# Kernel optimization log

Measured on AMD Instinct MI355X. Metric: run time of the kernel, lower is better.

The kernel has to match this reference:

```python
import jax, jax.numpy as jnp
import numpy as np

N = 50000      # nodes
E = 800000     # edges (avg degree 16)
NF, EF, H, OUT, K = 16, 8, 64, 8, 3
N_MID = 2      # n_gnn_layers=4 -> first + 2 mid + last


def setup_inputs() -> dict:
    key = jax.random.key(0)
    ks = jax.random.split(key, 16)
    s = 0.05
    return {
        "x": jax.random.normal(ks[0], (N, NF), dtype=jnp.float32),
        "edge_index": jax.random.randint(ks[1], (2, E), 0, N, dtype=jnp.int64),
        "edge_attr": jax.random.normal(ks[2], (E, EF), dtype=jnp.float32),
        # edge_aggr MLP: Linear(EF,H) -> ReLU -> Linear(H,1)
        "mlp_W1": jax.random.normal(ks[3], (EF, H), dtype=jnp.float32) * s,
        "mlp_b1": jnp.zeros((H,), dtype=jnp.float32),
        "mlp_W2": jax.random.normal(ks[4], (H, 1), dtype=jnp.float32) * s,
        "mlp_b2": jnp.zeros((1,), dtype=jnp.float32),
        # TAGConv-style layers: K+1 linear maps each
        "W_first": jax.random.normal(ks[5], (K + 1, NF, H), dtype=jnp.float32) * s,
        "b_first": jnp.zeros((H,), dtype=jnp.float32),
        "W_mid": jax.random.normal(ks[6], (N_MID, K + 1, H, H), dtype=jnp.float32) * s,
        "b_mid": jnp.zeros((N_MID, H), dtype=jnp.float32),
        "W_last": jax.random.normal(ks[7], (K + 1, H, OUT), dtype=jnp.float32) * s,
        "b_last": jnp.zeros((OUT,), dtype=jnp.float32),
    }


def _gcn_norm(edge_weight, src, dst, n_nodes):
    # deg computed at target (col), D^{-1/2} A D^{-1/2}, no self loops
    deg = jax.ops.segment_sum(edge_weight, dst, num_segments=n_nodes)
    dinv = jnp.where(deg > 0, jax.lax.rsqrt(jnp.where(deg > 0, deg, 1.0)), 0.0)
    return dinv[src] * edge_weight * dinv[dst]  # [E]


def _tag_conv(x, Ws, b, src, dst, norm, n_nodes):
    # out = sum_k (A_norm^k x) W_k + b
    out = x @ Ws[0]
    h = x
    for k in range(1, Ws.shape[0]):
        h = jax.ops.segment_sum(h[src] * norm[:, None], dst, num_segments=n_nodes)
        out = out + h @ Ws[k]
    return out + b


def reference(x, edge_index, edge_attr, mlp_W1, mlp_b1, mlp_W2, mlp_b2,
              W_first, b_first, W_mid, b_mid, W_last, b_last):
    src, dst = edge_index[0], edge_index[1]
    n_nodes = x.shape[0]
    # edge MLP -> scalar edge weight per edge
    ew = (jax.nn.relu(edge_attr @ mlp_W1 + mlp_b1) @ mlp_W2 + mlp_b2)[:, 0]  # [E]
    norm = _gcn_norm(ew, src, dst, n_nodes)
    h = jax.nn.relu(_tag_conv(x, W_first, b_first, src, dst, norm, n_nodes))
    for i in range(W_mid.shape[0]):
        h = jax.nn.relu(_tag_conv(h, W_mid[i], b_mid[i], src, dst, norm, n_nodes))
    return _tag_conv(h, W_last, b_last, src, dst, norm, n_nodes)
```

## Files before the change

kernel.cpp:

```cpp
#include <hip/hip_runtime.h>
#include <stdint.h>

#define N_NODES 50000
#define N_EDGES 800000
#define NFEAT   16
#define EFEAT   8
#define HID     64
#define OUTF    8
#define NMID    2
#define NX      (N_NODES * NFEAT)
#define NPW     16
#define CAP     64
#define PGB     ((N_NODES + 4 * NPW - 1) / (4 * NPW))
#define PPB     ((N_NODES + 15) / 16)
#define NWB     ((N_NODES + 3) / 4)

typedef unsigned short ushort_t;
typedef unsigned int   uint_t;
typedef unsigned long long ull_t;
typedef __bf16 bf16x8 __attribute__((ext_vector_type(8)));
typedef float  f32x4  __attribute__((ext_vector_type(4)));

__device__ __forceinline__ float b2f(ushort_t u) {
    return __uint_as_float(((uint_t)u) << 16);
}
__device__ __forceinline__ ushort_t f2b(float f) {
    uint_t u = __float_as_uint(f);
    return (ushort_t)((u + 0x7fffu + ((u >> 16) & 1u)) >> 16);
}
__device__ __forceinline__ float h2f(ushort_t u) {
    union { ushort_t u; _Float16 h; } c; c.u = u; return (float)c.h;
}
__device__ __forceinline__ ushort_t f2h(float f) {
    union { ushort_t u; _Float16 h; } c; c.h = (_Float16)f; return c.u;
}

__global__ __launch_bounds__(256) void edge_mlp_kernel(
    const float* __restrict__ ea, const float* __restrict__ x,
    const int* __restrict__ ei,
    const float* __restrict__ W1, const float* __restrict__ b1,
    const float* __restrict__ W2, const float* __restrict__ b2,
    ushort_t* __restrict__ xb,
    int* __restrict__ cnts, ull_t* __restrict__ bucket8)
{
    int tid = threadIdx.x;
    int e = blockIdx.x * 256 + tid;
    if (e >= N_EDGES) return;

    int d = ei[N_EDGES + e];
    int pos = atomicAdd(&cnts[d], 1);
    int sn = ei[e];

    xb[e] = f2b(x[e]);

    float4 v0 = ((const float4*)ea)[2 * e];
    float4 v1 = ((const float4*)ea)[2 * e + 1];
    float a[8] = {v0.x, v0.y, v0.z, v0.w, v1.x, v1.y, v1.z, v1.w};

    float h[HID];
    #pragma unroll
    for (int j = 0; j < HID; ++j) h[j] = b1[j];

    #pragma unroll
    for (int i = 0; i < EFEAT; ++i) {
        float ai = a[i];
        #pragma unroll
        for (int j = 0; j < HID; ++j)
            h[j] = fmaf(ai, W1[i * HID + j], h[j]);
    }

    float acc = b2[0];
    #pragma unroll
    for (int j = 0; j < HID; ++j)
        acc = fmaf(fmaxf(h[j], 0.f), W2[j], acc);

    if (pos < CAP)
        bucket8[(size_t)d * CAP + pos] =
            (((ull_t)__float_as_uint(acc)) << 32) | (uint_t)sn;
}

__global__ __launch_bounds__(256) void degdinv_kernel(
    int* __restrict__ cnts, const ull_t* __restrict__ bucket8,
    float* __restrict__ dinv)
{
    int tid = threadIdx.x;
    int n = blockIdx.x * 4 + (tid >> 6);
    int lane = tid & 63;
    if (n >= N_NODES) return;
    int c = cnts[n]; if (c > CAP) c = CAP;
    float w = 0.f;
    if (lane < c)
        w = __uint_as_float((uint_t)(bucket8[(size_t)n * CAP + lane] >> 32));
    #pragma unroll
    for (int o = 32; o; o >>= 1) w += __shfl_down(w, o, 64);
    if (lane == 0) {
        cnts[n] = c;
        dinv[n] = (w > 0.f) ? (1.f / sqrtf(w)) : 0.f;
    }
}

__global__ __launch_bounds__(256) void rescale_kernel(
    const int* __restrict__ cnts, const float* __restrict__ dinv,
    const ull_t* __restrict__ bucket8, uint_t* __restrict__ bucket4)
{
    int tid = threadIdx.x;
    int n = blockIdx.x * 4 + (tid >> 6);
    int lane = tid & 63;
    if (n >= N_NODES) return;
    int c = cnts[n];
    float dn = dinv[n];
    if (lane < c) {
        ull_t q = bucket8[(size_t)n * CAP + lane];
        uint_t s = (uint_t)q;
        float ewv = __uint_as_float((uint_t)(q >> 32));
        float nv = dinv[s] * ewv * dn;
        nv = fminf(fmaxf(nv, -60000.f), 60000.f);
        bucket4[(size_t)n * CAP + lane] = (((uint_t)f2h(nv)) << 16) | s;
    }
}

template<int W>
__global__ __launch_bounds__(256, 6) void prop_kernel(
    const ushort_t* __restrict__ gsrc, ushort_t* __restrict__ gout,
    const int* __restrict__ cnts, const uint_t* __restrict__ bucket)
{
    int tid = threadIdx.x;
    int wv = tid >> 6, lane = tid & 63;
    int nb = (blockIdx.x * 4 + wv) * 4;
    if (nb >= N_NODES) return;

    int cv = (lane < 4) ? cnts[nb + lane] : 0;
    int c0 = __builtin_amdgcn_readlane(cv, 0);
    int c1 = __builtin_amdgcn_readlane(cv, 1);
    int c2 = __builtin_amdgcn_readlane(cv, 2);
    int c3 = __builtin_amdgcn_readlane(cv, 3);
    int cm = max(max(c0, c1), max(c2, c3));

    uint_t p0 = 0, p1 = 0, p2 = 0, p3 = 0;
    if (lane < c0) p0 = bucket[(size_t)(nb + 0) * CAP + lane];
    if (lane < c1) p1 = bucket[(size_t)(nb + 1) * CAP + lane];
    if (lane < c2) p2 = bucket[(size_t)(nb + 2) * CAP + lane];
    if (lane < c3) p3 = bucket[(size_t)(nb + 3) * CAP + lane];

    if (W == 64) {
        float s[4][4];
        #pragma unroll
        for (int n = 0; n < 4; ++n)
            #pragma unroll
            for (int k = 0; k < 4; ++k) s[n][k] = 0.f;

        for (int j = 0; j < cm; j += 4) {
            float hv[4][4], nv[4][4];
            #pragma unroll
            for (int k = 0; k < 4; ++k) {
                int pe0 = __builtin_amdgcn_readlane((int)p0, j + k);
                int pe1 = __builtin_amdgcn_readlane((int)p1, j + k);
                int pe2 = __builtin_amdgcn_readlane((int)p2, j + k);
                int pe3 = __builtin_amdgcn_readlane((int)p3, j + k);
                nv[0][k] = h2f((ushort_t)(((uint_t)pe0) >> 16));
                nv[1][k] = h2f((ushort_t)(((uint_t)pe1) >> 16));
                nv[2][k] = h2f((ushort_t)(((uint_t)pe2) >> 16));
                nv[3][k] = h2f((ushort_t)(((uint_t)pe3) >> 16));
                hv[0][k] = b2f(gsrc[(size_t)(pe0 & 0xffff) * 64 + lane]);
                hv[1][k] = b2f(gsrc[(size_t)(pe1 & 0xffff) * 64 + lane]);
                hv[2][k] = b2f(gsrc[(size_t)(pe2 & 0xffff) * 64 + lane]);
                hv[3][k] = b2f(gsrc[(size_t)(pe3 & 0xffff) * 64 + lane]);
            }
            #pragma unroll
            for (int n = 0; n < 4; ++n)
                #pragma unroll
                for (int k = 0; k < 4; ++k)
                    s[n][k] = fmaf(hv[n][k], nv[n][k], s[n][k]);
        }

        #pragma unroll
        for (int n = 0; n < 4; ++n) {
            float v = (s[n][0] + s[n][1]) + (s[n][2] + s[n][3]);
            gout[(size_t)(nb + n) * 64 + lane] = f2b(v);
        }
    } else {
        const int il = lane & 15;
        const int quad = lane >> 4;
        float s0 = 0.f, s1 = 0.f, s2 = 0.f, s3 = 0.f;

        #pragma unroll 2
        for (int j = 0; j < cm; j += 4) {
            int jq = j + quad;
            int w0 = __shfl((int)p0, jq, 64);
            int w1 = __shfl((int)p1, jq, 64);
            int w2 = __shfl((int)p2, jq, 64);
            int w3 = __shfl((int)p3, jq, 64);
            float h0 = b2f(gsrc[(size_t)(w0 & 0xffff) * 16 + il]);
            float h1 = b2f(gsrc[(size_t)(w1 & 0xffff) * 16 + il]);
            float h2 = b2f(gsrc[(size_t)(w2 & 0xffff) * 16 + il]);
            float h3 = b2f(gsrc[(size_t)(w3 & 0xffff) * 16 + il]);
            s0 = fmaf(h0, h2f((ushort_t)(((uint_t)w0) >> 16)), s0);
            s1 = fmaf(h1, h2f((ushort_t)(((uint_t)w1) >> 16)), s1);
            s2 = fmaf(h2, h2f((ushort_t)(((uint_t)w2) >> 16)), s2);
            s3 = fmaf(h3, h2f((ushort_t)(((uint_t)w3) >> 16)), s3);
        }

        s0 += __shfl_xor(s0, 16, 64); s0 += __shfl_xor(s0, 32, 64);
        s1 += __shfl_xor(s1, 16, 64); s1 += __shfl_xor(s1, 32, 64);
        s2 += __shfl_xor(s2, 16, 64); s2 += __shfl_xor(s2, 32, 64);
        s3 += __shfl_xor(s3, 16, 64); s3 += __shfl_xor(s3, 32, 64);
        if (lane < 16) {
            gout[(size_t)(nb + 0) * 16 + lane] = f2b(s0);
            gout[(size_t)(nb + 1) * 16 + lane] = f2b(s1);
            gout[(size_t)(nb + 2) * 16 + lane] = f2b(s2);
            gout[(size_t)(nb + 3) * 16 + lane] = f2b(s3);
        }
    }
}

template<int F32OUT>
__global__ __launch_bounds__(256, 8) void prop8_kernel(
    const ushort_t* __restrict__ gsrc, int GS, int GO,
    const ushort_t* __restrict__ add, int AS, int AO,
    ushort_t* __restrict__ outb, float* __restrict__ outf,
    const int* __restrict__ cnts, const uint_t* __restrict__ bucket)
{
    int tid = threadIdx.x;
    int wv = tid >> 6, lane = tid & 63;
    int nb = (blockIdx.x * 4 + wv) * 4;
    if (nb >= N_NODES) return;
    const int oct = lane >> 3, il = lane & 7;

    int cv = (lane < 4) ? cnts[nb + lane] : 0;
    int c0 = __builtin_amdgcn_readlane(cv, 0);
    int c1 = __builtin_amdgcn_readlane(cv, 1);
    int c2 = __builtin_amdgcn_readlane(cv, 2);
    int c3 = __builtin_amdgcn_readlane(cv, 3);
    int cm = max(max(c0, c1), max(c2, c3));

    uint_t p0 = 0, p1 = 0, p2 = 0, p3 = 0;
    if (lane < c0) p0 = bucket[(size_t)(nb + 0) * CAP + lane];
    if (lane < c1) p1 = bucket[(size_t)(nb + 1) * CAP + lane];
    if (lane < c2) p2 = bucket[(size_t)(nb + 2) * CAP + lane];
    if (lane < c3) p3 = bucket[(size_t)(nb + 3) * CAP + lane];

    float s0 = 0.f, s1 = 0.f, s2 = 0.f, s3 = 0.f;

    #pragma unroll 2
    for (int j = 0; j < cm; j += 8) {
        int jo = j + oct;
        int w0 = __shfl((int)p0, jo, 64);
        int w1 = __shfl((int)p1, jo, 64);
        int w2 = __shfl((int)p2, jo, 64);
        int w3 = __shfl((int)p3, jo, 64);
        float h0 = b2f(gsrc[(size_t)(w0 & 0xffff) * GS + GO + il]);
        float h1 = b2f(gsrc[(size_t)(w1 & 0xffff) * GS + GO + il]);
        float h2 = b2f(gsrc[(size_t)(w2 & 0xffff) * GS + GO + il]);
        float h3 = b2f(gsrc[(size_t)(w3 & 0xffff) * GS + GO + il]);
        s0 = fmaf(h0, h2f((ushort_t)(((uint_t)w0) >> 16)), s0);
        s1 = fmaf(h1, h2f((ushort_t)(((uint_t)w1) >> 16)), s1);
        s2 = fmaf(h2, h2f((ushort_t)(((uint_t)w2) >> 16)), s2);
        s3 = fmaf(h3, h2f((ushort_t)(((uint_t)w3) >> 16)), s3);
    }

    #define FIN(sN, n)                                                               \
        {                                                                            \
            float s = sN;                                                            \
            s += __shfl_xor(s, 8, 64);                                               \
            s += __shfl_xor(s, 16, 64);                                              \
            s += __shfl_xor(s, 32, 64);                                              \
            if (lane < 8) {                                                          \
                float v = s + b2f(add[(size_t)(nb + n) * AS + AO + lane]);           \
                if (F32OUT) outf[(size_t)(nb + n) * 8 + lane] = v;                   \
                else        outb[(size_t)(nb + n) * 8 + lane] = f2b(v);              \
            }                                                                        \
        }
    FIN(s0, 0)
    FIN(s1, 1)
    FIN(s2, 2)
    FIN(s3, 3)
    #undef FIN
}

template<int SRCW, int COUT, int ACT>
__global__ __launch_bounds__(256, 4) void gemm4_kernel(
    const ushort_t* __restrict__ s0, const ushort_t* __restrict__ s1,
    const ushort_t* __restrict__ s2, const ushort_t* __restrict__ s3,
    const float* __restrict__ Wg,
    const float* __restrict__ bias,
    ushort_t* __restrict__ outb)
{
    constexpr int NCH = (SRCW == 16) ? 2 : 8;
    constexpr int NT  = (COUT + 15) / 16;
    __shared__ __align__(16) ushort_t Bp[NCH * NT * 512];

    int tid = threadIdx.x;
    for (int idx = tid; idx < NCH * NT * 512; idx += 256) {
        int f = idx >> 9;
        int l = (idx >> 3) & 63, j = idx & 7;
        int ch = f / NT, nt = f - ch * NT;
        int kk = ((l >> 4) << 3) + j;
        int n = nt * 16 + (l & 15);
        int widx, krow;
        if (SRCW == 16) { widx = 2 * ch + (kk >> 4); krow = kk & 15; }
        else            { widx = ch >> 1;            krow = ((ch & 1) << 5) + kk; }
        float v = (n < COUT) ? Wg[((size_t)widx * SRCW + krow) * COUT + n] : 0.f;
        Bp[idx] = f2b(v);
    }
    __syncthreads();

    int wv = tid >> 6, lane = tid & 63;
    int node_base = (blockIdx.x * 4 + wv) * NPW;
    if (node_base >= N_NODES) return;
    int m = lane & 15, quad = lane >> 4;

    const ushort_t* srcs[4] = {s0, s1, s2, s3};
    bf16x8 a[NCH];
    #pragma unroll
    for (int ch = 0; ch < NCH; ++ch) {
        const ushort_t* sp;
        size_t off;
        if (SRCW == 16) {
            sp = (quad < 2) ? srcs[2 * ch] : srcs[2 * ch + 1];
            off = (size_t)(node_base + m) * 16 + (quad & 1) * 8;
        } else {
            sp = srcs[ch >> 1];
            off = (size_t)(node_base + m) * 64 + ((ch & 1) << 5) + quad * 8;
        }
        a[ch] = *(const bf16x8*)(sp + off);
    }

    #pragma unroll
    for (int nt = 0; nt < NT; ++nt) {
        float bv = bias[(nt * 16 + m) & (COUT - 1)];
        f32x4 c = {bv, bv, bv, bv};
        #pragma unroll
        for (int ch = 0; ch < NCH; ++ch) {
            bf16x8 b = *(const bf16x8*)&Bp[((ch * NT + nt) * 64 + lane) * 8];
            c = __builtin_amdgcn_mfma_f32_16x16x32_bf16(a[ch], b, c, 0, 0, 0);
        }
        #pragma unroll
        for (int r = 0; r < 4; ++r) {
            int row = node_base + quad * 4 + r;
            float v = ACT ? fmaxf(c[r], 0.f) : c[r];
            outb[(size_t)row * COUT + nt * 16 + m] = f2b(v);
        }
    }
}

__global__ __launch_bounds__(256, 4) void gemmL_kernel(
    const ushort_t* __restrict__ src,
    const float* __restrict__ Wl,
    const float* __restrict__ bl,
    ushort_t* __restrict__ Z)
{
    __shared__ __align__(16) ushort_t Bp[2 * 2 * 512];

    int tid = threadIdx.x;
    for (int idx = tid; idx < 2048; idx += 256) {
        int f = idx >> 9;
        int ch = f >> 1, nt = f & 1;
        int l = (idx >> 3) & 63, j = idx & 7;
        int kg = ch * 32 + ((l >> 4) << 3) + j;
        int n = nt * 16 + (l & 15);
        int widx = n >> 3, col = n & 7;
        Bp[idx] = f2b(Wl[((size_t)widx * 64 + kg) * 8 + col]);
    }
    __syncthreads();

    int wv = tid >> 6, lane = tid & 63;
    int node_base = (blockIdx.x * 4 + wv) * NPW;
    if (node_base >= N_NODES) return;
    int m = lane & 15, quad = lane >> 4;

    bf16x8 a[2];
    #pragma unroll
    for (int ch = 0; ch < 2; ++ch)
        a[ch] = *(const bf16x8*)(src + (size_t)(node_base + m) * 64 + ch * 32 + quad * 8);

    #pragma unroll
    for (int nt = 0; nt < 2; ++nt) {
        int n = nt * 16 + m;
        float bv = (n < 8) ? bl[n] : 0.f;
        f32x4 c = {bv, bv, bv, bv};
        #pragma unroll
        for (int ch = 0; ch < 2; ++ch) {
            bf16x8 b = *(const bf16x8*)&Bp[((ch * 2 + nt) * 64 + lane) * 8];
            c = __builtin_amdgcn_mfma_f32_16x16x32_bf16(a[ch], b, c, 0, 0, 0);
        }
        #pragma unroll
        for (int r = 0; r < 4; ++r) {
            int row = node_base + quad * 4 + r;
            Z[(size_t)row * 32 + n] = f2b(c[r]);
        }
    }
}

extern "C" void kernel_launch(void* const* d_in, const int* in_sizes, int n_in,
                              void* d_out, int out_size, void* d_ws, size_t ws_size,
                              hipStream_t stream)
{
    const float* x  = (const float*)d_in[0];
    const int*   ei = (const int*)d_in[1];
    const float* ea = (const float*)d_in[2];
    const float* W1 = (const float*)d_in[3];
    const float* b1 = (const float*)d_in[4];
    const float* W2 = (const float*)d_in[5];
    const float* b2 = (const float*)d_in[6];
    const float* Wf = (const float*)d_in[7];
    const float* bf = (const float*)d_in[8];
    const float* Wm = (const float*)d_in[9];
    const float* bm = (const float*)d_in[10];
    const float* Wl = (const float*)d_in[11];
    const float* bl = (const float*)d_in[12];

    char* ws = (char*)d_ws;
    size_t off = 0;
    auto take = [&](size_t bytes) -> char* {
        char* p = ws + off;
        off = (off + bytes + 255) & ~(size_t)255;
        return p;
    };
    int*      cnts    = (int*)take((size_t)N_NODES * 4);
    float*    dinv    = (float*)take((size_t)N_NODES * 4);
    ull_t*    bucket8 = (ull_t*)take((size_t)N_NODES * CAP * 8);
    uint_t*   bucket4 = (uint_t*)take((size_t)N_NODES * CAP * 4);
    ushort_t* xb      = (ushort_t*)take((size_t)NX * 2 + 256);
    ushort_t* g1      = (ushort_t*)take((size_t)N_NODES * HID * 2 + 256);
    ushort_t* g2      = (ushort_t*)take((size_t)N_NODES * HID * 2 + 256);
    ushort_t* g3      = (ushort_t*)take((size_t)N_NODES * HID * 2 + 256);
    ushort_t* curA    = (ushort_t*)take((size_t)N_NODES * HID * 2 + 256);
    ushort_t* curB    = (ushort_t*)take((size_t)N_NODES * HID * 2 + 256);
    ushort_t* Z       = (ushort_t*)take((size_t)N_NODES * 32 * 2 + 256);
    ushort_t* t8a     = (ushort_t*)take((size_t)N_NODES * 8 * 2 + 256);
    ushort_t* t8b     = (ushort_t*)take((size_t)N_NODES * 8 * 2 + 256);

    hipMemsetAsync(cnts, 0, (size_t)N_NODES * 4, stream);

    const int EB = (N_EDGES + 255) / 256;

    edge_mlp_kernel<<<EB, 256, 0, stream>>>(ea, x, ei, W1, b1, W2, b2, xb, cnts, bucket8);
    degdinv_kernel<<<NWB, 256, 0, stream>>>(cnts, bucket8, dinv);
    rescale_kernel<<<NWB, 256, 0, stream>>>(cnts, dinv, bucket8, bucket4);

    prop_kernel<NFEAT><<<PPB, 256, 0, stream>>>(xb, g1, cnts, bucket4);
    prop_kernel<NFEAT><<<PPB, 256, 0, stream>>>(g1, g2, cnts, bucket4);
    prop_kernel<NFEAT><<<PPB, 256, 0, stream>>>(g2, g3, cnts, bucket4);
    gemm4_kernel<NFEAT, HID, 1><<<PGB, 256, 0, stream>>>(
        xb, g1, g2, g3, Wf, bf, curA);

    ushort_t* cin = curA;
    ushort_t* cot = curB;
    for (int L = 0; L < NMID; ++L) {
        prop_kernel<HID><<<PPB, 256, 0, stream>>>(cin, g1, cnts, bucket4);
        prop_kernel<HID><<<PPB, 256, 0, stream>>>(g1, g2, cnts, bucket4);
        prop_kernel<HID><<<PPB, 256, 0, stream>>>(g2, g3, cnts, bucket4);
        gemm4_kernel<HID, HID, 1><<<PGB, 256, 0, stream>>>(
            cin, g1, g2, g3, Wm + (size_t)L * 4 * HID * HID, bm + L * HID, cot);
        ushort_t* t = cin; cin = cot; cot = t;
    }

    gemmL_kernel<<<PGB, 256, 0, stream>>>(cin, Wl, bl, Z);
    prop8_kernel<0><<<PPB, 256, 0, stream>>>(Z, 32, 24, Z, 32, 16, t8a, nullptr, cnts, bucket4);
    prop8_kernel<0><<<PPB, 256, 0, stream>>>(t8a, 8, 0, Z, 32, 8, t8b, nullptr, cnts, bucket4);
    prop8_kernel<1><<<PPB, 256, 0, stream>>>(t8b, 8, 0, Z, 32, 0, nullptr, (float*)d_out, cnts, bucket4);
}
```

Baseline: 414.4 us.

## Restructure prop kernel lanes to gather 4 bf16 columns per lane

Rewrites the propagation kernel's lane mapping so each 16-lane group of a wave handles one of the four nodes. Each lane gathers 4 bf16 features with one 8-byte vector load, and bucket entries are spread across lanes and broadcast by shuffle instead of readlane. The aim is fewer, wider gather loads and less per-edge scalar overhead. The W=16 path also changes its reduction pattern. The occupancy hint in launch_bounds is dropped. The cost is a per-node serial loop bounded by the wave's max degree, and possible register growth without the occupancy hint.

```diff
diff --git a/kernel.cpp b/kernel.cpp
--- a/kernel.cpp
+++ b/kernel.cpp
@@ -120,7 +120,7 @@
 }
 
 template<int W>
-__global__ __launch_bounds__(256, 6) void prop_kernel(
+__global__ __launch_bounds__(256) void prop_kernel(
     const ushort_t* __restrict__ gsrc, ushort_t* __restrict__ gout,
     const int* __restrict__ cnts, const uint_t* __restrict__ bucket)
 {
@@ -129,86 +129,114 @@
     int nb = (blockIdx.x * 4 + wv) * 4;
     if (nb >= N_NODES) return;
 
+    int nsel = lane >> 4;
     int cv = (lane < 4) ? cnts[nb + lane] : 0;
     int c0 = __builtin_amdgcn_readlane(cv, 0);
     int c1 = __builtin_amdgcn_readlane(cv, 1);
     int c2 = __builtin_amdgcn_readlane(cv, 2);
     int c3 = __builtin_amdgcn_readlane(cv, 3);
     int cm = max(max(c0, c1), max(c2, c3));
-
-    uint_t p0 = 0, p1 = 0, p2 = 0, p3 = 0;
-    if (lane < c0) p0 = bucket[(size_t)(nb + 0) * CAP + lane];
-    if (lane < c1) p1 = bucket[(size_t)(nb + 1) * CAP + lane];
-    if (lane < c2) p2 = bucket[(size_t)(nb + 2) * CAP + lane];
-    if (lane < c3) p3 = bucket[(size_t)(nb + 3) * CAP + lane];
+    int cmy = (nsel == 0) ? c0 : (nsel == 1) ? c1 : (nsel == 2) ? c2 : c3;
+
+    int es = lane & 15;
+    const uint_t* bb = bucket + (size_t)(nb + nsel) * CAP + es;
+    uint_t q0 = (es      < cmy) ? bb[0]  : 0u;
+    uint_t q1 = (es + 16 < cmy) ? bb[16] : 0u;
+    uint_t q2 = (es + 32 < cmy) ? bb[32] : 0u;
+    uint_t q3 = (es + 48 < cmy) ? bb[48] : 0u;
+
+    int bidx = lane & 48;
 
     if (W == 64) {
-        float s[4][4];
-        #pragma unroll
-        for (int n = 0; n < 4; ++n)
+        const int colg = (lane & 15) * 4;
+        const ushort_t* gbase = gsrc + colg;
+        float s0 = 0.f, s1 = 0.f, s2 = 0.f, s3 = 0.f;
+
+        #define STEP64(QR, T)                                                        \
+            {                                                                        \
+                int w = __shfl((int)QR, bidx + (T), 64);                             \
+                float nv = h2f((ushort_t)(((uint_t)w) >> 16));                       \
+                uint2 d = *(const uint2*)(gbase + (size_t)(w & 0xffff) * 64);        \
+                s0 = fmaf(__uint_as_float(d.x << 16), nv, s0);                       \
+                s1 = fmaf(__uint_as_float(d.x & 0xffff0000u), nv, s1);               \
+                s2 = fmaf(__uint_as_float(d.y << 16), nv, s2);                       \
+                s3 = fmaf(__uint_as_float(d.y & 0xffff0000u), nv, s3);               \
+            }
+
+        {
+            int lim = cm < 16 ? cm : 16;
+            #pragma unroll 4
+            for (int t = 0; t < lim; ++t) STEP64(q0, t)
+        }
+        if (cm > 16) {
+            int lim = cm - 16; if (lim > 16) lim = 16;
+            #pragma unroll 4
+            for (int t = 0; t < lim; ++t) STEP64(q1, t)
+        }
+        if (cm > 32) {
+            int lim = cm - 32; if (lim > 16) lim = 16;
+            #pragma unroll 4
+            for (int t = 0; t < lim; ++t) STEP64(q2, t)
+        }
+        if (cm > 48) {
+            int lim = cm - 48; if (lim > 16) lim = 16;
+            #pragma unroll 4
+            for (int t = 0; t < lim; ++t) STEP64(q3, t)
+        }
+        #undef STEP64
+
+        uint2 o;
+        o.x = (uint_t)f2b(s0) | (((uint_t)f2b(s1)) << 16);
+        o.y = (uint_t)f2b(s2) | (((uint_t)f2b(s3)) << 16);
+        *(uint2*)(gout + (size_t)(nb + nsel) * 64 + colg) = o;
+    } else {
+        const int qg = (lane >> 2) & 3;
+        const int colg = (lane & 3) * 4;
+        const ushort_t* gbase = gsrc + colg;
+        float s0 = 0.f, s1 = 0.f, s2 = 0.f, s3 = 0.f;
+
+        #define STEP16(QR, T)                                                        \
+            {                                                                        \
+                int w = __shfl((int)QR, bidx + (T) + qg, 64);                        \
+                float nv = h2f((ushort_t)(((uint_t)w) >> 16));                       \
+                uint2 d = *(const uint2*)(gbase + (size_t)(w & 0xffff) * 16);        \
+                s0 = fmaf(__uint_as_float(d.x << 16), nv, s0);                       \
+                s1 = fmaf(__uint_as_float(d.x & 0xffff0000u), nv, s1);               \
+                s2 = fmaf(__uint_as_float(d.y << 16), nv, s2);                       \
+                s3 = fmaf(__uint_as_float(d.y & 0xffff0000u), nv, s3);               \
+            }
+
+        {
+            int lim = cm < 16 ? cm : 16;
             #pragma unroll
-            for (int k = 0; k < 4; ++k) s[n][k] = 0.f;
-
-        for (int j = 0; j < cm; j += 4) {
-            float hv[4][4], nv[4][4];
+            for (int t = 0; t < 16; t += 4) { if (t < lim) STEP16(q0, t) }
+        }
+        if (cm > 16) {
+            int lim = cm - 16; if (lim > 16) lim = 16;
             #pragma unroll
-            for (int k = 0; k < 4; ++k) {
-                int pe0 = __builtin_amdgcn_readlane((int)p0, j + k);
-                int pe1 = __builtin_amdgcn_readlane((int)p1, j + k);
-                int pe2 = __builtin_amdgcn_readlane((int)p2, j + k);
-                int pe3 = __builtin_amdgcn_readlane((int)p3, j + k);
-                nv[0][k] = h2f((ushort_t)(((uint_t)pe0) >> 16));
-                nv[1][k] = h2f((ushort_t)(((uint_t)pe1) >> 16));
-                nv[2][k] = h2f((ushort_t)(((uint_t)pe2) >> 16));
-                nv[3][k] = h2f((ushort_t)(((uint_t)pe3) >> 16));
-                hv[0][k] = b2f(gsrc[(size_t)(pe0 & 0xffff) * 64 + lane]);
-                hv[1][k] = b2f(gsrc[(size_t)(pe1 & 0xffff) * 64 + lane]);
-                hv[2][k] = b2f(gsrc[(size_t)(pe2 & 0xffff) * 64 + lane]);
-                hv[3][k] = b2f(gsrc[(size_t)(pe3 & 0xffff) * 64 + lane]);
-            }
+            for (int t = 0; t < 16; t += 4) { if (t < lim) STEP16(q1, t) }
+        }
+        if (cm > 32) {
+            int lim = cm - 32; if (lim > 16) lim = 16;
             #pragma unroll
-            for (int n = 0; n < 4; ++n)
-                #pragma unroll
-                for (int k = 0; k < 4; ++k)
-                    s[n][k] = fmaf(hv[n][k], nv[n][k], s[n][k]);
-        }
-
-        #pragma unroll
-        for (int n = 0; n < 4; ++n) {
-            float v = (s[n][0] + s[n][1]) + (s[n][2] + s[n][3]);
-            gout[(size_t)(nb + n) * 64 + lane] = f2b(v);
-        }
-    } else {
-        const int il = lane & 15;
-        const int quad = lane >> 4;
-        float s0 = 0.f, s1 = 0.f, s2 = 0.f, s3 = 0.f;
-
-        #pragma unroll 2
-        for (int j = 0; j < cm; j += 4) {
-            int jq = j + quad;
-            int w0 = __shfl((int)p0, jq, 64);
-            int w1 = __shfl((int)p1, jq, 64);
-            int w2 = __shfl((int)p2, jq, 64);
-            int w3 = __shfl((int)p3, jq, 64);
-            float h0 = b2f(gsrc[(size_t)(w0 & 0xffff) * 16 + il]);
-            float h1 = b2f(gsrc[(size_t)(w1 & 0xffff) * 16 + il]);
-            float h2 = b2f(gsrc[(size_t)(w2 & 0xffff) * 16 + il]);
-            float h3 = b2f(gsrc[(size_t)(w3 & 0xffff) * 16 + il]);
-            s0 = fmaf(h0, h2f((ushort_t)(((uint_t)w0) >> 16)), s0);
-            s1 = fmaf(h1, h2f((ushort_t)(((uint_t)w1) >> 16)), s1);
-            s2 = fmaf(h2, h2f((ushort_t)(((uint_t)w2) >> 16)), s2);
-            s3 = fmaf(h3, h2f((ushort_t)(((uint_t)w3) >> 16)), s3);
-        }
-
-        s0 += __shfl_xor(s0, 16, 64); s0 += __shfl_xor(s0, 32, 64);
-        s1 += __shfl_xor(s1, 16, 64); s1 += __shfl_xor(s1, 32, 64);
-        s2 += __shfl_xor(s2, 16, 64); s2 += __shfl_xor(s2, 32, 64);
-        s3 += __shfl_xor(s3, 16, 64); s3 += __shfl_xor(s3, 32, 64);
-        if (lane < 16) {
-            gout[(size_t)(nb + 0) * 16 + lane] = f2b(s0);
-            gout[(size_t)(nb + 1) * 16 + lane] = f2b(s1);
-            gout[(size_t)(nb + 2) * 16 + lane] = f2b(s2);
-            gout[(size_t)(nb + 3) * 16 + lane] = f2b(s3);
+            for (int t = 0; t < 16; t += 4) { if (t < lim) STEP16(q2, t) }
+        }
+        if (cm > 48) {
+            int lim = cm - 48; if (lim > 16) lim = 16;
+            #pragma unroll
+            for (int t = 0; t < 16; t += 4) { if (t < lim) STEP16(q3, t) }
+        }
+        #undef STEP16
+
+        s0 += __shfl_xor(s0, 4, 64); s0 += __shfl_xor(s0, 8, 64);
+        s1 += __shfl_xor(s1, 4, 64); s1 += __shfl_xor(s1, 8, 64);
+        s2 += __shfl_xor(s2, 4, 64); s2 += __shfl_xor(s2, 8, 64);
+        s3 += __shfl_xor(s3, 4, 64); s3 += __shfl_xor(s3, 8, 64);
+        if ((lane & 12) == 0) {
+            uint2 o;
+            o.x = (uint_t)f2b(s0) | (((uint_t)f2b(s1)) << 16);
+            o.y = (uint_t)f2b(s2) | (((uint_t)f2b(s3)) << 16);
+            *(uint2*)(gout + (size_t)(nb + nsel) * 16 + colg) = o;
         }
     }
 }
```

Result: no change. 412.4 us (-0.5%).

## Split 64-wide hidden features into two 32-column halves for propagation

Applied to the files above, without the earlier changes.

Hidden-layer feature arrays are stored as two separate 32-column bf16 halves, so each 64-wide propagation becomes two passes of a 32-wide gather kernel. Each half table is 3.2 MB rather than 6.4 MB, which is meant to keep the randomly gathered source rows resident in cache. Bucket loads and output stores in the new kernel use nontemporal hints. The GEMM kernels are specialized to read and write the split halves. The cost is twice as many propagation launches and the edge-list bucket being read twice per hop.

```diff
diff --git a/kernel.cpp b/kernel.cpp
--- a/kernel.cpp
+++ b/kernel.cpp
@@ -119,8 +119,7 @@
     }
 }
 
-template<int W>
-__global__ __launch_bounds__(256, 6) void prop_kernel(
+__global__ __launch_bounds__(256, 6) void prop16_kernel(
     const ushort_t* __restrict__ gsrc, ushort_t* __restrict__ gout,
     const int* __restrict__ cnts, const uint_t* __restrict__ bucket)
 {
@@ -142,74 +141,91 @@
     if (lane < c2) p2 = bucket[(size_t)(nb + 2) * CAP + lane];
     if (lane < c3) p3 = bucket[(size_t)(nb + 3) * CAP + lane];
 
-    if (W == 64) {
-        float s[4][4];
-        #pragma unroll
-        for (int n = 0; n < 4; ++n)
-            #pragma unroll
-            for (int k = 0; k < 4; ++k) s[n][k] = 0.f;
-
-        for (int j = 0; j < cm; j += 4) {
-            float hv[4][4], nv[4][4];
-            #pragma unroll
-            for (int k = 0; k < 4; ++k) {
-                int pe0 = __builtin_amdgcn_readlane((int)p0, j + k);
-                int pe1 = __builtin_amdgcn_readlane((int)p1, j + k);
-                int pe2 = __builtin_amdgcn_readlane((int)p2, j + k);
-                int pe3 = __builtin_amdgcn_readlane((int)p3, j + k);
-                nv[0][k] = h2f((ushort_t)(((uint_t)pe0) >> 16));
-                nv[1][k] = h2f((ushort_t)(((uint_t)pe1) >> 16));
-                nv[2][k] = h2f((ushort_t)(((uint_t)pe2) >> 16));
-                nv[3][k] = h2f((ushort_t)(((uint_t)pe3) >> 16));
-                hv[0][k] = b2f(gsrc[(size_t)(pe0 & 0xffff) * 64 + lane]);
-                hv[1][k] = b2f(gsrc[(size_t)(pe1 & 0xffff) * 64 + lane]);
-                hv[2][k] = b2f(gsrc[(size_t)(pe2 & 0xffff) * 64 + lane]);
-                hv[3][k] = b2f(gsrc[(size_t)(pe3 & 0xffff) * 64 + lane]);
-            }
-            #pragma unroll
-            for (int n = 0; n < 4; ++n)
-                #pragma unroll
-                for (int k = 0; k < 4; ++k)
-                    s[n][k] = fmaf(hv[n][k], nv[n][k], s[n][k]);
-        }
-
-        #pragma unroll
-        for (int n = 0; n < 4; ++n) {
-            float v = (s[n][0] + s[n][1]) + (s[n][2] + s[n][3]);
-            gout[(size_t)(nb + n) * 64 + lane] = f2b(v);
-        }
-    } else {
-        const int il = lane & 15;
-        const int quad = lane >> 4;
-        float s0 = 0.f, s1 = 0.f, s2 = 0.f, s3 = 0.f;
-
-        #pragma unroll 2
-        for (int j = 0; j < cm; j += 4) {
-            int jq = j + quad;
-            int w0 = __shfl((int)p0, jq, 64);
-            int w1 = __shfl((int)p1, jq, 64);
-            int w2 = __shfl((int)p2, jq, 64);
-            int w3 = __shfl((int)p3, jq, 64);
-            float h0 = b2f(gsrc[(size_t)(w0 & 0xffff) * 16 + il]);
-            float h1 = b2f(gsrc[(size_t)(w1 & 0xffff) * 16 + il]);
-            float h2 = b2f(gsrc[(size_t)(w2 & 0xffff) * 16 + il]);
-            float h3 = b2f(gsrc[(size_t)(w3 & 0xffff) * 16 + il]);
-            s0 = fmaf(h0, h2f((ushort_t)(((uint_t)w0) >> 16)), s0);
-            s1 = fmaf(h1, h2f((ushort_t)(((uint_t)w1) >> 16)), s1);
-            s2 = fmaf(h2, h2f((ushort_t)(((uint_t)w2) >> 16)), s2);
-            s3 = fmaf(h3, h2f((ushort_t)(((uint_t)w3) >> 16)), s3);
-        }
-
-        s0 += __shfl_xor(s0, 16, 64); s0 += __shfl_xor(s0, 32, 64);
-        s1 += __shfl_xor(s1, 16, 64); s1 += __shfl_xor(s1, 32, 64);
-        s2 += __shfl_xor(s2, 16, 64); s2 += __shfl_xor(s2, 32, 64);
-        s3 += __shfl_xor(s3, 16, 64); s3 += __shfl_xor(s3, 32, 64);
-        if (lane < 16) {
-            gout[(size_t)(nb + 0) * 16 + lane] = f2b(s0);
-            gout[(size_t)(nb + 1) * 16 + lane] = f2b(s1);
-            gout[(size_t)(nb + 2) * 16 + lane] = f2b(s2);
-            gout[(size_t)(nb + 3) * 16 + lane] = f2b(s3);
-        }
+    const int il = lane & 15;
+    const int quad = lane >> 4;
+    float s0 = 0.f, s1 = 0.f, s2 = 0.f, s3 = 0.f;
+
+    #pragma unroll 2
+    for (int j = 0; j < cm; j += 4) {
+        int jq = j + quad;
+        int w0 = __shfl((int)p0, jq, 64);
+        int w1 = __shfl((int)p1, jq, 64);
+        int w2 = __shfl((int)p2, jq, 64);
+        int w3 = __shfl((int)p3, jq, 64);
+        float h0 = b2f(gsrc[(size_t)(w0 & 0xffff) * 16 + il]);
+        float h1 = b2f(gsrc[(size_t)(w1 & 0xffff) * 16 + il]);
+        float h2 = b2f(gsrc[(size_t)(w2 & 0xffff) * 16 + il]);
+        float h3 = b2f(gsrc[(size_t)(w3 & 0xffff) * 16 + il]);
+        s0 = fmaf(h0, h2f((ushort_t)(((uint_t)w0) >> 16)), s0);
+        s1 = fmaf(h1, h2f((ushort_t)(((uint_t)w1) >> 16)), s1);
+        s2 = fmaf(h2, h2f((ushort_t)(((uint_t)w2) >> 16)), s2);
+        s3 = fmaf(h3, h2f((ushort_t)(((uint_t)w3) >> 16)), s3);
+    }
+
+    s0 += __shfl_xor(s0, 16, 64); s0 += __shfl_xor(s0, 32, 64);
+    s1 += __shfl_xor(s1, 16, 64); s1 += __shfl_xor(s1, 32, 64);
+    s2 += __shfl_xor(s2, 16, 64); s2 += __shfl_xor(s2, 32, 64);
+    s3 += __shfl_xor(s3, 16, 64); s3 += __shfl_xor(s3, 32, 64);
+    if (lane < 16) {
+        gout[(size_t)(nb + 0) * 16 + lane] = f2b(s0);
+        gout[(size_t)(nb + 1) * 16 + lane] = f2b(s1);
+        gout[(size_t)(nb + 2) * 16 + lane] = f2b(s2);
+        gout[(size_t)(nb + 3) * 16 + lane] = f2b(s3);
+    }
+}
+
+__global__ __launch_bounds__(256, 6) void prop32_kernel(
+    const ushort_t* __restrict__ gsrc, ushort_t* __restrict__ gout,
+    const int* __restrict__ cnts, const uint_t* __restrict__ bucket)
+{
+    int tid = threadIdx.x;
+    int wv = tid >> 6, lane = tid & 63;
+    int nb = (blockIdx.x * 4 + wv) * 4;
+    if (nb >= N_NODES) return;
+
+    int cv = (lane < 4) ? cnts[nb + lane] : 0;
+    int c0 = __builtin_amdgcn_readlane(cv, 0);
+    int c1 = __builtin_amdgcn_readlane(cv, 1);
+    int c2 = __builtin_amdgcn_readlane(cv, 2);
+    int c3 = __builtin_amdgcn_readlane(cv, 3);
+    int cm = max(max(c0, c1), max(c2, c3));
+
+    uint_t p0 = 0, p1 = 0, p2 = 0, p3 = 0;
+    if (lane < c0) p0 = __builtin_nontemporal_load(&bucket[(size_t)(nb + 0) * CAP + lane]);
+    if (lane < c1) p1 = __builtin_nontemporal_load(&bucket[(size_t)(nb + 1) * CAP + lane]);
+    if (lane < c2) p2 = __builtin_nontemporal_load(&bucket[(size_t)(nb + 2) * CAP + lane]);
+    if (lane < c3) p3 = __builtin_nontemporal_load(&bucket[(size_t)(nb + 3) * CAP + lane]);
+
+    const int il = lane & 31;
+    const int pr = lane >> 5;
+    float s0 = 0.f, s1 = 0.f, s2 = 0.f, s3 = 0.f;
+
+    #pragma unroll 4
+    for (int j = 0; j < cm; j += 2) {
+        int jq = j + pr;
+        int w0 = __shfl((int)p0, jq, 64);
+        int w1 = __shfl((int)p1, jq, 64);
+        int w2 = __shfl((int)p2, jq, 64);
+        int w3 = __shfl((int)p3, jq, 64);
+        float h0 = b2f(gsrc[(size_t)(w0 & 0xffff) * 32 + il]);
+        float h1 = b2f(gsrc[(size_t)(w1 & 0xffff) * 32 + il]);
+        float h2 = b2f(gsrc[(size_t)(w2 & 0xffff) * 32 + il]);
+        float h3 = b2f(gsrc[(size_t)(w3 & 0xffff) * 32 + il]);
+        s0 = fmaf(h0, h2f((ushort_t)(((uint_t)w0) >> 16)), s0);
+        s1 = fmaf(h1, h2f((ushort_t)(((uint_t)w1) >> 16)), s1);
+        s2 = fmaf(h2, h2f((ushort_t)(((uint_t)w2) >> 16)), s2);
+        s3 = fmaf(h3, h2f((ushort_t)(((uint_t)w3) >> 16)), s3);
+    }
+
+    s0 += __shfl_xor(s0, 32, 64);
+    s1 += __shfl_xor(s1, 32, 64);
+    s2 += __shfl_xor(s2, 32, 64);
+    s3 += __shfl_xor(s3, 32, 64);
+    if (lane < 32) {
+        __builtin_nontemporal_store(f2b(s0), &gout[(size_t)(nb + 0) * 32 + il]);
+        __builtin_nontemporal_store(f2b(s1), &gout[(size_t)(nb + 1) * 32 + il]);
+        __builtin_nontemporal_store(f2b(s2), &gout[(size_t)(nb + 2) * 32 + il]);
+        __builtin_nontemporal_store(f2b(s3), &gout[(size_t)(nb + 3) * 32 + il]);
     }
 }
 
@@ -277,16 +293,15 @@
     #undef FIN
 }
 
-template<int SRCW, int COUT, int ACT>
-__global__ __launch_bounds__(256, 4) void gemm4_kernel(
+template<int ACT>
+__global__ __launch_bounds__(256, 4) void gemm4_16_kernel(
     const ushort_t* __restrict__ s0, const ushort_t* __restrict__ s1,
     const ushort_t* __restrict__ s2, const ushort_t* __restrict__ s3,
     const float* __restrict__ Wg,
     const float* __restrict__ bias,
-    ushort_t* __restrict__ outb)
-{
-    constexpr int NCH = (SRCW == 16) ? 2 : 8;
-    constexpr int NT  = (COUT + 15) / 16;
+    ushort_t* __restrict__ outA, ushort_t* __restrict__ outB)
+{
+    constexpr int NCH = 2, NT = 4;
     __shared__ __align__(16) ushort_t Bp[NCH * NT * 512];
 
     int tid = threadIdx.x;
@@ -296,11 +311,8 @@
         int ch = f / NT, nt = f - ch * NT;
         int kk = ((l >> 4) << 3) + j;
         int n = nt * 16 + (l & 15);
-        int widx, krow;
-        if (SRCW == 16) { widx = 2 * ch + (kk >> 4); krow = kk & 15; }
-        else            { widx = ch >> 1;            krow = ((ch & 1) << 5) + kk; }
-        float v = (n < COUT) ? Wg[((size_t)widx * SRCW + krow) * COUT + n] : 0.f;
-        Bp[idx] = f2b(v);
+        int widx = 2 * ch + (kk >> 4), krow = kk & 15;
+        Bp[idx] = f2b(Wg[((size_t)widx * NFEAT + krow) * HID + n]);
     }
     __syncthreads();
 
@@ -313,38 +325,88 @@
     bf16x8 a[NCH];
     #pragma unroll
     for (int ch = 0; ch < NCH; ++ch) {
-        const ushort_t* sp;
-        size_t off;
-        if (SRCW == 16) {
-            sp = (quad < 2) ? srcs[2 * ch] : srcs[2 * ch + 1];
-            off = (size_t)(node_base + m) * 16 + (quad & 1) * 8;
-        } else {
-            sp = srcs[ch >> 1];
-            off = (size_t)(node_base + m) * 64 + ((ch & 1) << 5) + quad * 8;
-        }
-        a[ch] = *(const bf16x8*)(sp + off);
+        const ushort_t* sp = (quad < 2) ? srcs[2 * ch] : srcs[2 * ch + 1];
+        a[ch] = *(const bf16x8*)(sp + (size_t)(node_base + m) * 16 + (quad & 1) * 8);
     }
 
     #pragma unroll
     for (int nt = 0; nt < NT; ++nt) {
-        float bv = bias[(nt * 16 + m) & (COUT - 1)];
+        float bv = bias[nt * 16 + m];
         f32x4 c = {bv, bv, bv, bv};
         #pragma unroll
         for (int ch = 0; ch < NCH; ++ch) {
             bf16x8 b = *(const bf16x8*)&Bp[((ch * NT + nt) * 64 + lane) * 8];
             c = __builtin_amdgcn_mfma_f32_16x16x32_bf16(a[ch], b, c, 0, 0, 0);
         }
+        ushort_t* oh = (nt >> 1) ? outB : outA;
+        int col = (nt & 1) * 16 + m;
         #pragma unroll
         for (int r = 0; r < 4; ++r) {
             int row = node_base + quad * 4 + r;
             float v = ACT ? fmaxf(c[r], 0.f) : c[r];
-            outb[(size_t)row * COUT + nt * 16 + m] = f2b(v);
+            oh[(size_t)row * 32 + col] = f2b(v);
+        }
+    }
+}
+
+template<int ACT>
+__global__ __launch_bounds__(256, 4) void gemm4_32_kernel(
+    const ushort_t* __restrict__ s0a, const ushort_t* __restrict__ s0b,
+    const ushort_t* __restrict__ s1a, const ushort_t* __restrict__ s1b,
+    const ushort_t* __restrict__ s2a, const ushort_t* __restrict__ s2b,
+    const ushort_t* __restrict__ s3a, const ushort_t* __restrict__ s3b,
+    const float* __restrict__ Wg,
+    const float* __restrict__ bias,
+    ushort_t* __restrict__ outA, ushort_t* __restrict__ outB)
+{
+    constexpr int NCH = 8, NT = 4;
+    __shared__ __align__(16) ushort_t Bp[NCH * NT * 512];
+
+    int tid = threadIdx.x;
+    for (int idx = tid; idx < NCH * NT * 512; idx += 256) {
+        int f = idx >> 9;
+        int l = (idx >> 3) & 63, j = idx & 7;
+        int ch = f / NT, nt = f - ch * NT;
+        int kk = ((l >> 4) << 3) + j;
+        int n = nt * 16 + (l & 15);
+        int widx = ch >> 1, krow = ((ch & 1) << 5) + kk;
+        Bp[idx] = f2b(Wg[((size_t)widx * HID + krow) * HID + n]);
+    }
+    __syncthreads();
+
+    int wv = tid >> 6, lane = tid & 63;
+    int node_base = (blockIdx.x * 4 + wv) * NPW;
+    if (node_base >= N_NODES) return;
+    int m = lane & 15, quad = lane >> 4;
+
+    const ushort_t* const srcs[8] = {s0a, s0b, s1a, s1b, s2a, s2b, s3a, s3b};
+    bf16x8 a[NCH];
+    #pragma unroll
+    for (int ch = 0; ch < NCH; ++ch)
+        a[ch] = *(const bf16x8*)(srcs[ch] + (size_t)(node_base + m) * 32 + quad * 8);
+
+    #pragma unroll
+    for (int nt = 0; nt < NT; ++nt) {
+        float bv = bias[nt * 16 + m];
+        f32x4 c = {bv, bv, bv, bv};
+        #pragma unroll
+        for (int ch = 0; ch < NCH; ++ch) {
+            bf16x8 b = *(const bf16x8*)&Bp[((ch * NT + nt) * 64 + lane) * 8];
+            c = __builtin_amdgcn_mfma_f32_16x16x32_bf16(a[ch], b, c, 0, 0, 0);
+        }
+        ushort_t* oh = (nt >> 1) ? outB : outA;
+        int col = (nt & 1) * 16 + m;
+        #pragma unroll
+        for (int r = 0; r < 4; ++r) {
+            int row = node_base + quad * 4 + r;
+            float v = ACT ? fmaxf(c[r], 0.f) : c[r];
+            oh[(size_t)row * 32 + col] = f2b(v);
         }
     }
 }
 
 __global__ __launch_bounds__(256, 4) void gemmL_kernel(
-    const ushort_t* __restrict__ src,
+    const ushort_t* __restrict__ srcA, const ushort_t* __restrict__ srcB,
     const float* __restrict__ Wl,
     const float* __restrict__ bl,
     ushort_t* __restrict__ Z)
@@ -369,9 +431,8 @@
     int m = lane & 15, quad = lane >> 4;
 
     bf16x8 a[2];
-    #pragma unroll
-    for (int ch = 0; ch < 2; ++ch)
-        a[ch] = *(const bf16x8*)(src + (size_t)(node_base + m) * 64 + ch * 32 + quad * 8);
+    a[0] = *(const bf16x8*)(srcA + (size_t)(node_base + m) * 32 + quad * 8);
+    a[1] = *(const bf16x8*)(srcB + (size_t)(node_base + m) * 32 + quad * 8);
 
     #pragma unroll
     for (int nt = 0; nt < 2; ++nt) {
@@ -421,11 +482,19 @@
     ull_t*    bucket8 = (ull_t*)take((size_t)N_NODES * CAP * 8);
     uint_t*   bucket4 = (uint_t*)take((size_t)N_NODES * CAP * 4);
     ushort_t* xb      = (ushort_t*)take((size_t)NX * 2 + 256);
-    ushort_t* g1      = (ushort_t*)take((size_t)N_NODES * HID * 2 + 256);
-    ushort_t* g2      = (ushort_t*)take((size_t)N_NODES * HID * 2 + 256);
-    ushort_t* g3      = (ushort_t*)take((size_t)N_NODES * HID * 2 + 256);
-    ushort_t* curA    = (ushort_t*)take((size_t)N_NODES * HID * 2 + 256);
-    ushort_t* curB    = (ushort_t*)take((size_t)N_NODES * HID * 2 + 256);
+    ushort_t* g1w     = (ushort_t*)take((size_t)N_NODES * 16 * 2 + 256);
+    ushort_t* g2w     = (ushort_t*)take((size_t)N_NODES * 16 * 2 + 256);
+    ushort_t* g3w     = (ushort_t*)take((size_t)N_NODES * 16 * 2 + 256);
+    ushort_t* h1a     = (ushort_t*)take((size_t)N_NODES * 32 * 2 + 256);
+    ushort_t* h1b     = (ushort_t*)take((size_t)N_NODES * 32 * 2 + 256);
+    ushort_t* h2a     = (ushort_t*)take((size_t)N_NODES * 32 * 2 + 256);
+    ushort_t* h2b     = (ushort_t*)take((size_t)N_NODES * 32 * 2 + 256);
+    ushort_t* h3a     = (ushort_t*)take((size_t)N_NODES * 32 * 2 + 256);
+    ushort_t* h3b     = (ushort_t*)take((size_t)N_NODES * 32 * 2 + 256);
+    ushort_t* curAa   = (ushort_t*)take((size_t)N_NODES * 32 * 2 + 256);
+    ushort_t* curAb   = (ushort_t*)take((size_t)N_NODES * 32 * 2 + 256);
+    ushort_t* curBa   = (ushort_t*)take((size_t)N_NODES * 32 * 2 + 256);
+    ushort_t* curBb   = (ushort_t*)take((size_t)N_NODES * 32 * 2 + 256);
     ushort_t* Z       = (ushort_t*)take((size_t)N_NODES * 32 * 2 + 256);
     ushort_t* t8a     = (ushort_t*)take((size_t)N_NODES * 8 * 2 + 256);
     ushort_t* t8b     = (ushort_t*)take((size_t)N_NODES * 8 * 2 + 256);
@@ -438,24 +507,30 @@
     degdinv_kernel<<<NWB, 256, 0, stream>>>(cnts, bucket8, dinv);
     rescale_kernel<<<NWB, 256, 0, stream>>>(cnts, dinv, bucket8, bucket4);
 
-    prop_kernel<NFEAT><<<PPB, 256, 0, stream>>>(xb, g1, cnts, bucket4);
-    prop_kernel<NFEAT><<<PPB, 256, 0, stream>>>(g1, g2, cnts, bucket4);
-    prop_kernel<NFEAT><<<PPB, 256, 0, stream>>>(g2, g3, cnts, bucket4);
-    gemm4_kernel<NFEAT, HID, 1><<<PGB, 256, 0, stream>>>(
-        xb, g1, g2, g3, Wf, bf, curA);
-
-    ushort_t* cin = curA;
-    ushort_t* cot = curB;
+    prop16_kernel<<<PPB, 256, 0, stream>>>(xb, g1w, cnts, bucket4);
+    prop16_kernel<<<PPB, 256, 0, stream>>>(g1w, g2w, cnts, bucket4);
+    prop16_kernel<<<PPB, 256, 0, stream>>>(g2w, g3w, cnts, bucket4);
+    gemm4_16_kernel<1><<<PGB, 256, 0, stream>>>(
+        xb, g1w, g2w, g3w, Wf, bf, curAa, curAb);
+
+    ushort_t* cinA = curAa; ushort_t* cinB = curAb;
+    ushort_t* cotA = curBa; ushort_t* cotB = curBb;
     for (int L = 0; L < NMID; ++L) {
-        prop_kernel<HID><<<PPB, 256, 0, stream>>>(cin, g1, cnts, bucket4);
-        prop_kernel<HID><<<PPB, 256, 0, stream>>>(g1, g2, cnts, bucket4);
-        prop_kernel<HID><<<PPB, 256, 0, stream>>>(g2, g3, cnts, bucket4);
-        gemm4_kernel<HID, HID, 1><<<PGB, 256, 0, stream>>>(
-            cin, g1, g2, g3, Wm + (size_t)L * 4 * HID * HID, bm + L * HID, cot);
-        ushort_t* t = cin; cin = cot; cot = t;
-    }
-
-    gemmL_kernel<<<PGB, 256, 0, stream>>>(cin, Wl, bl, Z);
+        prop32_kernel<<<PPB, 256, 0, stream>>>(cinA, h1a, cnts, bucket4);
+        prop32_kernel<<<PPB, 256, 0, stream>>>(cinB, h1b, cnts, bucket4);
+        prop32_kernel<<<PPB, 256, 0, stream>>>(h1a, h2a, cnts, bucket4);
+        prop32_kernel<<<PPB, 256, 0, stream>>>(h1b, h2b, cnts, bucket4);
+        prop32_kernel<<<PPB, 256, 0, stream>>>(h2a, h3a, cnts, bucket4);
+        prop32_kernel<<<PPB, 256, 0, stream>>>(h2b, h3b, cnts, bucket4);
+        gemm4_32_kernel<1><<<PGB, 256, 0, stream>>>(
+            cinA, cinB, h1a, h1b, h2a, h2b, h3a, h3b,
+            Wm + (size_t)L * 4 * HID * HID, bm + L * HID, cotA, cotB);
+        ushort_t* t;
+        t = cinA; cinA = cotA; cotA = t;
+        t = cinB; cinB = cotB; cotB = t;
+    }
+
+    gemmL_kernel<<<PGB, 256, 0, stream>>>(cinA, cinB, Wl, bl, Z);
     prop8_kernel<0><<<PPB, 256, 0, stream>>>(Z, 32, 24, Z, 32, 16, t8a, nullptr, cnts, bucket4);
     prop8_kernel<0><<<PPB, 256, 0, stream>>>(t8a, 8, 0, Z, 32, 8, t8b, nullptr, cnts, bucket4);
     prop8_kernel<1><<<PPB, 256, 0, stream>>>(t8b, 8, 0, Z, 32, 0, nullptr, (float*)d_out, cnts, bucket4);
```

Result: slower. 464.0 us (+12.0%).
